# Optimization experiments

Hardware: AMD Instinct MI355X
Metric: run time of the kernel (lower is better)

## Reference

```python
import jax, jax.numpy as jnp
import numpy as np
import math

STRIDES = {"p3": 8, "p4": 16, "p5": 32}
STRIDE_SCALE = 4
ASPECT_RATIOS = (0.5, 1.0, 2.0)
IOU_THRESH = (0.3, 0.7)
SCALE_CLAMP = math.log(224.0 / 8.0)
IMG_SIZE = 640.0


def _make_locations(key, hw, stride):
    # random centers within image, roughly on the stride grid scale
    return jax.random.uniform(key, (hw, 2), dtype=jnp.float32) * (IMG_SIZE - stride) + stride / 2


def setup_inputs() -> dict:
    key = jax.random.key(0)
    ks = jax.random.split(key, 8)
    locations_p3 = _make_locations(ks[0], 6400, 8)
    locations_p4 = _make_locations(ks[1], 1600, 16)
    locations_p5 = _make_locations(ks[2], 400, 32)
    deltas_p3 = jax.random.normal(ks[3], (19200, 4), dtype=jnp.float32) * 0.2
    deltas_p4 = jax.random.normal(ks[4], (4800, 4), dtype=jnp.float32) * 0.2
    deltas_p5 = jax.random.normal(ks[5], (1200, 4), dtype=jnp.float32) * 0.2
    # GT boxes: (M,5) valid xyxy + class label
    M = 64
    xy = jax.random.uniform(ks[6], (M, 2), dtype=jnp.float32) * (IMG_SIZE - 64.0)
    wh = jax.random.uniform(ks[7], (M, 2), dtype=jnp.float32) * 128.0 + 16.0
    cls = jnp.ones((M, 1), dtype=jnp.float32)
    gt_boxes = jnp.concatenate([xy, jnp.minimum(xy + wh, IMG_SIZE), cls], axis=1)
    return {
        "locations_p3": locations_p3, "locations_p4": locations_p4, "locations_p5": locations_p5,
        "deltas_p3": deltas_p3, "deltas_p4": deltas_p4, "deltas_p5": deltas_p5,
        "gt_boxes": gt_boxes,
    }


def generate_anchors(locations, stride):
    # locations: (HW, 2) centers -> (HW*A, 4) XYXY anchors
    area = float((stride * STRIDE_SCALE) ** 2)
    boxes = []
    for ar in ASPECT_RATIOS:
        w = math.sqrt(area / ar)
        h = area / w
        half = jnp.array([w / 2, h / 2], dtype=jnp.float32)
        boxes.append(jnp.concatenate([locations - half, locations + half], axis=1))
    # stack per-location: (HW, A, 4) -> (HW*A, 4)
    return jnp.stack(boxes, axis=1).reshape(-1, 4)


def apply_deltas(deltas, anchors):
    tx, ty = deltas[:, 0], deltas[:, 1]
    tw = jnp.minimum(deltas[:, 2], SCALE_CLAMP)
    th = jnp.minimum(deltas[:, 3], SCALE_CLAMP)
    px = (anchors[:, 0] + anchors[:, 2]) / 2
    py = (anchors[:, 1] + anchors[:, 3]) / 2
    pw = jnp.abs(anchors[:, 0] - anchors[:, 2])
    ph = jnp.abs(anchors[:, 1] - anchors[:, 3])
    bx = px + pw * tx
    by = py + ph * ty
    bw = pw * jnp.exp(tw)
    bh = ph * jnp.exp(th)
    # NOTE: original code has y2 = by + bw/2 (bug preserved for faithfulness)
    return jnp.stack([bx - bw / 2, by - bh / 2, bx + bw / 2, by + bw / 2], axis=1)


def iou_matrix(boxes1, boxes2):
    # boxes1: (M,4), boxes2: (N,4) -> (M,N)
    b1 = boxes1[:, None, :]
    b2 = boxes2[None, :, :]
    area1 = jnp.abs((b1[..., 0] - b1[..., 2]) * (b1[..., 1] - b1[..., 3]))
    area2 = jnp.abs((b2[..., 0] - b2[..., 2]) * (b2[..., 1] - b2[..., 3]))
    xl = jnp.maximum(b1[..., 0], b2[..., 0])
    yb = jnp.maximum(b1[..., 1], b2[..., 1])
    xr = jnp.minimum(b1[..., 2], b2[..., 2])
    yt = jnp.minimum(b1[..., 3], b2[..., 3])
    no_int = (xl > xr) | (yb > yt)
    inter = jnp.abs((xl - xr) * (yb - yt))
    iou = inter / (area1 + area2 - inter)
    return jnp.where(no_int, 0.0, iou)


def match_anchors_to_gt(anchors, gt_boxes):
    # anchors (N,4), gt_boxes (M,5) -> matched (N,5)
    mm = iou_matrix(anchors, gt_boxes[:, :4])  # (N, M)
    matched_idx = jnp.argmax(mm, axis=1)
    quality = jnp.max(mm, axis=1)
    matched = gt_boxes[matched_idx]  # (N,5)
    lo, hi = IOU_THRESH
    matched = jnp.where((quality <= lo)[:, None], -1.0, matched)
    neutral = (quality > lo) & (quality < hi)
    matched = jnp.where(neutral[:, None], -1e8, matched)
    return matched


def get_deltas_from_anchors(anchors, matched_gt):
    px = (anchors[:, 0] + anchors[:, 2]) / 2
    py = (anchors[:, 1] + anchors[:, 3]) / 2
    pw = jnp.abs(anchors[:, 0] - anchors[:, 2])
    ph = jnp.abs(anchors[:, 1] - anchors[:, 3])
    bx = (matched_gt[:, 0] + matched_gt[:, 2]) / 2
    by = (matched_gt[:, 1] + matched_gt[:, 3]) / 2
    bw = jnp.abs(matched_gt[:, 0] - matched_gt[:, 2])
    bh = jnp.abs(matched_gt[:, 1] - matched_gt[:, 3])
    tx = (bx - px) / pw
    ty = (by - py) / ph
    tw = jnp.log(jnp.maximum(bw, 1e-12) / pw)
    th = jnp.log(jnp.maximum(bh, 1e-12) / ph)
    deltas = jnp.stack([tx, ty, tw, th], axis=1)
    excluded = matched_gt[:, 4] < 0
    return jnp.where(excluded[:, None], -1e8, deltas)


def reference(locations_p3, locations_p4, locations_p5,
              deltas_p3, deltas_p4, deltas_p5, gt_boxes):
    a3 = generate_anchors(locations_p3, STRIDES["p3"])
    a4 = generate_anchors(locations_p4, STRIDES["p4"])
    a5 = generate_anchors(locations_p5, STRIDES["p5"])
    anchors = jnp.concatenate([a3, a4, a5], axis=0)  # (N,4)
    deltas = jnp.concatenate([deltas_p3, deltas_p4, deltas_p5], axis=0)
    proposals = apply_deltas(deltas, anchors)  # decoded boxes (N,4)
    matched_gt = match_anchors_to_gt(anchors, gt_boxes)  # (N,5)
    gt_deltas = get_deltas_from_anchors(anchors, matched_gt)  # (N,4)
    return proposals, matched_gt, gt_deltas
```

## Files before the change

kernel.cpp:

```cpp
#include <hip/hip_runtime.h>
#include <math.h>

#define NP3 19200
#define NP4 4800
#define NP5 1200
#define NA  (NP3 + NP4 + NP5)
#define MGT 64

#define SCALE_CLAMP_F 3.3322045101752038f
#define NEG_BIG (-100000000.0f)

__constant__ float c_half[3][3][2] = {
    {{22.62741699796952f, 11.313708498984761f},
     {16.0f, 16.0f},
     {11.313708498984761f, 22.62741699796952f}},
    {{45.25483399593904f, 22.62741699796952f},
     {32.0f, 32.0f},
     {22.62741699796952f, 45.25483399593904f}},
    {{90.50966799187808f, 45.25483399593904f},
     {64.0f, 64.0f},
     {45.25483399593904f, 90.50966799187808f}},
};

__global__ __launch_bounds__(256)
void rpn_fused_kernel(const float* __restrict__ loc3,
                      const float* __restrict__ loc4,
                      const float* __restrict__ loc5,
                      const float* __restrict__ del3,
                      const float* __restrict__ del4,
                      const float* __restrict__ del5,
                      const float* __restrict__ gt,
                      float* __restrict__ out)
{
    __shared__ float sg0[MGT], sg1[MGT], sg2[MGT], sg3[MGT], sg4[MGT], sa2[MGT];
    const int t = threadIdx.x;
    if (t < MGT) {
        const float g0 = gt[t * 5 + 0];
        const float g1 = gt[t * 5 + 1];
        const float g2 = gt[t * 5 + 2];
        const float g3 = gt[t * 5 + 3];
        const float g4 = gt[t * 5 + 4];
        sg0[t] = g0; sg1[t] = g1; sg2[t] = g2; sg3[t] = g3; sg4[t] = g4;
        sa2[t] = fabsf((g0 - g2) * (g1 - g3));
    }
    __syncthreads();

    const int sub = t & 3;
    const int a = blockIdx.x * 64 + (t >> 2);
    if (a >= NA) return;

    int lvl, rel;
    const float* locs;
    const float* dels;
    if (a < NP3)              { lvl = 0; rel = a;              locs = loc3; dels = del3; }
    else if (a < NP3 + NP4)   { lvl = 1; rel = a - NP3;        locs = loc4; dels = del4; }
    else                      { lvl = 2; rel = a - NP3 - NP4;  locs = loc5; dels = del5; }

    const int li = rel / 3;
    const int ar = rel - li * 3;

    const float lx = locs[li * 2 + 0];
    const float ly = locs[li * 2 + 1];
    const float hw = c_half[lvl][ar][0];
    const float hh = c_half[lvl][ar][1];
    const float x0 = lx - hw, y0 = ly - hh;
    const float x1 = lx + hw, y1 = ly + hh;

    const float px = (x0 + x1) * 0.5f;
    const float py = (y0 + y1) * 0.5f;
    const float pw = fabsf(x0 - x1);
    const float ph = fabsf(y0 - y1);
    const float area1 = fabsf((x0 - x1) * (y0 - y1));

    float bi = -1.0f, bu = 1.0f;
    int   bj = sub * 16;
    const int j0 = sub * 16;
    #pragma unroll
    for (int i = 0; i < 16; ++i) {
        const int j = j0 + i;
        const float g0 = sg0[j];
        const float g1 = sg1[j];
        const float g2 = sg2[j];
        const float g3 = sg3[j];
        const float xl = fmaxf(x0, g0);
        const float yb = fmaxf(y0, g1);
        const float xr = fminf(x1, g2);
        const float yt = fminf(y1, g3);
        float inter = fabsf((xl - xr) * (yb - yt));
        if ((xl > xr) || (yb > yt)) inter = 0.0f;
        const float uni = (area1 + sa2[j]) - inter;
        const double c1 = (double)bi   * (double)uni;
        const double c2 = (double)inter * (double)bu;
        if (c2 > c1) { bi = inter; bu = uni; bj = j; }
    }

    #pragma unroll
    for (int m = 1; m <= 2; m <<= 1) {
        const float obi = __shfl_xor(bi, m, 64);
        const float obu = __shfl_xor(bu, m, 64);
        const int   obj = __shfl_xor(bj, m, 64);
        const double c1 = (double)bi  * (double)obu;
        const double c2 = (double)obi * (double)bu;
        if (c2 > c1 || (c2 == c1 && obj < bj)) { bi = obi; bu = obu; bj = obj; }
    }

    const float q = bi / bu;
    float m0 = sg0[bj], m1 = sg1[bj], m2 = sg2[bj], m3 = sg3[bj], m4 = sg4[bj];
    const double qd = (double)q;
    if (qd <= 0.3) {
        m0 = m1 = m2 = m3 = m4 = -1.0f;
    } else if (qd < 0.7) {
        m0 = m1 = m2 = m3 = m4 = NEG_BIG;
    }

    if (sub == 0) {
        const float tx = dels[rel * 4 + 0];
        const float ty = dels[rel * 4 + 1];
        const float tw = fminf(dels[rel * 4 + 2], SCALE_CLAMP_F);
        const float th = fminf(dels[rel * 4 + 3], SCALE_CLAMP_F);
        const float bx = px + pw * tx;
        const float by = py + ph * ty;
        const float bw = pw * expf(tw);
        const float bh = ph * expf(th);
        float4 prop;
        prop.x = bx - bw * 0.5f;
        prop.y = by - bh * 0.5f;
        prop.z = bx + bw * 0.5f;
        prop.w = by + bw * 0.5f;
        *reinterpret_cast<float4*>(out + (size_t)a * 4) = prop;
    } else if (sub == 1) {
        float* mout = out + (size_t)NA * 4 + (size_t)a * 5;
        mout[0] = m0; mout[1] = m1; mout[2] = m2; mout[3] = m3; mout[4] = m4;
    } else if (sub == 2) {
        float4 gd;
        if (m4 < 0.0f) {
            gd.x = gd.y = gd.z = gd.w = NEG_BIG;
        } else {
            const float bx = (m0 + m2) * 0.5f;
            const float by = (m1 + m3) * 0.5f;
            const float bw = fabsf(m0 - m2);
            const float bh = fabsf(m1 - m3);
            gd.x = (bx - px) / pw;
            gd.y = (by - py) / ph;
            gd.z = logf(fmaxf(bw, 1e-12f) / pw);
            gd.w = logf(fmaxf(bh, 1e-12f) / ph);
        }
        *reinterpret_cast<float4*>(out + (size_t)NA * 9 + (size_t)a * 4) = gd;
    }
}

extern "C" void kernel_launch(void* const* d_in, const int* in_sizes, int n_in,
                              void* d_out, int out_size, void* d_ws, size_t ws_size,
                              hipStream_t stream) {
    const float* loc3 = (const float*)d_in[0];
    const float* loc4 = (const float*)d_in[1];
    const float* loc5 = (const float*)d_in[2];
    const float* del3 = (const float*)d_in[3];
    const float* del4 = (const float*)d_in[4];
    const float* del5 = (const float*)d_in[5];
    const float* gt   = (const float*)d_in[6];
    float* out = (float*)d_out;

    const int grid = (NA + 63) / 64;
    rpn_fused_kernel<<<grid, 256, 0, stream>>>(loc3, loc4, loc5,
                                               del3, del4, del5, gt, out);
}
```

Baseline: 9.842 us.

## Split GT matching across 8 lanes per anchor with tree reduction and float4 LDS

Each anchor is now handled by 8 lanes instead of 4, so each lane scans 8 GT boxes rather than 16, and the grid doubles to 32 anchors per block. GT boxes are stored in shared memory as float4 so each is fetched with one LDS read. The serial running-max over IoU is replaced by a local pairwise tree reduction. The delta load is issued early as a single float4. This shortens the dependent chain of double-precision compares per thread, at the cost of twice as many blocks, an extra shuffle round and more lanes idle during the output stores.

```diff
diff --git a/kernel.cpp b/kernel.cpp
--- a/kernel.cpp
+++ b/kernel.cpp
@@ -32,21 +32,23 @@
                       const float* __restrict__ gt,
                       float* __restrict__ out)
 {
-    __shared__ float sg0[MGT], sg1[MGT], sg2[MGT], sg3[MGT], sg4[MGT], sa2[MGT];
+    __shared__ float4 sbox[MGT];
+    __shared__ float  sa2[MGT];
+    __shared__ float  scls[MGT];
     const int t = threadIdx.x;
     if (t < MGT) {
         const float g0 = gt[t * 5 + 0];
         const float g1 = gt[t * 5 + 1];
         const float g2 = gt[t * 5 + 2];
         const float g3 = gt[t * 5 + 3];
-        const float g4 = gt[t * 5 + 4];
-        sg0[t] = g0; sg1[t] = g1; sg2[t] = g2; sg3[t] = g3; sg4[t] = g4;
-        sa2[t] = fabsf((g0 - g2) * (g1 - g3));
+        sbox[t] = make_float4(g0, g1, g2, g3);
+        sa2[t]  = fabsf((g0 - g2) * (g1 - g3));
+        scls[t] = gt[t * 5 + 4];
     }
     __syncthreads();
 
-    const int sub = t & 3;
-    const int a = blockIdx.x * 64 + (t >> 2);
+    const int sub = t & 7;
+    const int a = blockIdx.x * 32 + (t >> 3);
     if (a >= NA) return;
 
     int lvl, rel;
@@ -58,6 +60,9 @@
 
     const int li = rel / 3;
     const int ar = rel - li * 3;
+
+    float4 del;
+    if (sub == 0) del = *reinterpret_cast<const float4*>(dels + (size_t)rel * 4);
 
     const float lx = locs[li * 2 + 0];
     const float ly = locs[li * 2 + 1];
@@ -72,30 +77,38 @@
     const float ph = fabsf(y0 - y1);
     const float area1 = fabsf((x0 - x1) * (y0 - y1));
 
-    float bi = -1.0f, bu = 1.0f;
-    int   bj = sub * 16;
-    const int j0 = sub * 16;
+    const int j0 = sub * 8;
+    float vi[8], vu[8];
+    int   vj[8];
     #pragma unroll
-    for (int i = 0; i < 16; ++i) {
+    for (int i = 0; i < 8; ++i) {
         const int j = j0 + i;
-        const float g0 = sg0[j];
-        const float g1 = sg1[j];
-        const float g2 = sg2[j];
-        const float g3 = sg3[j];
-        const float xl = fmaxf(x0, g0);
-        const float yb = fmaxf(y0, g1);
-        const float xr = fminf(x1, g2);
-        const float yt = fminf(y1, g3);
+        const float4 b = sbox[j];
+        const float xl = fmaxf(x0, b.x);
+        const float yb = fmaxf(y0, b.y);
+        const float xr = fminf(x1, b.z);
+        const float yt = fminf(y1, b.w);
         float inter = fabsf((xl - xr) * (yb - yt));
         if ((xl > xr) || (yb > yt)) inter = 0.0f;
-        const float uni = (area1 + sa2[j]) - inter;
-        const double c1 = (double)bi   * (double)uni;
-        const double c2 = (double)inter * (double)bu;
-        if (c2 > c1) { bi = inter; bu = uni; bj = j; }
+        vi[i] = inter;
+        vu[i] = (area1 + sa2[j]) - inter;
+        vj[i] = j;
     }
 
     #pragma unroll
-    for (int m = 1; m <= 2; m <<= 1) {
+    for (int s = 1; s < 8; s <<= 1) {
+        #pragma unroll
+        for (int k = 0; k < 8; k += 2 * s) {
+            const double cl = (double)vi[k]     * (double)vu[k + s];
+            const double cr = (double)vi[k + s] * (double)vu[k];
+            if (cr > cl) { vi[k] = vi[k + s]; vu[k] = vu[k + s]; vj[k] = vj[k + s]; }
+        }
+    }
+    float bi = vi[0], bu = vu[0];
+    int   bj = vj[0];
+
+    #pragma unroll
+    for (int m = 1; m <= 4; m <<= 1) {
         const float obi = __shfl_xor(bi, m, 64);
         const float obu = __shfl_xor(bu, m, 64);
         const int   obj = __shfl_xor(bj, m, 64);
@@ -105,7 +118,8 @@
     }
 
     const float q = bi / bu;
-    float m0 = sg0[bj], m1 = sg1[bj], m2 = sg2[bj], m3 = sg3[bj], m4 = sg4[bj];
+    const float4 mb = sbox[bj];
+    float m0 = mb.x, m1 = mb.y, m2 = mb.z, m3 = mb.w, m4 = scls[bj];
     const double qd = (double)q;
     if (qd <= 0.3) {
         m0 = m1 = m2 = m3 = m4 = -1.0f;
@@ -114,10 +128,10 @@
     }
 
     if (sub == 0) {
-        const float tx = dels[rel * 4 + 0];
-        const float ty = dels[rel * 4 + 1];
-        const float tw = fminf(dels[rel * 4 + 2], SCALE_CLAMP_F);
-        const float th = fminf(dels[rel * 4 + 3], SCALE_CLAMP_F);
+        const float tx = del.x;
+        const float ty = del.y;
+        const float tw = fminf(del.z, SCALE_CLAMP_F);
+        const float th = fminf(del.w, SCALE_CLAMP_F);
         const float bx = px + pw * tx;
         const float by = py + ph * ty;
         const float bw = pw * expf(tw);
@@ -161,7 +175,7 @@
     const float* gt   = (const float*)d_in[6];
     float* out = (float*)d_out;
 
-    const int grid = (NA + 63) / 64;
+    const int grid = (NA + 31) / 32;
     rpn_fused_kernel<<<grid, 256, 0, stream>>>(loc3, loc4, loc5,
                                                del3, del4, del5, gt, out);
 }
```

New measurement: 9.865 us. About the same (+0.2%).
